# Optimization experiments

Measured on AMD Instinct MI355X. Metric: run time of the kernel, lower is better.

Reference implementation:

```python
import jax, jax.numpy as jnp
import numpy as np

B, T, C, NH = 8, 1024, 1024, 16
DH = C // NH  # 64


def setup_inputs() -> dict:
    key = jax.random.key(0)
    ks = jax.random.split(key, 7)
    s = 1.0 / np.sqrt(C)
    return {
        "x": jax.random.normal(ks[0], (B, T, C), dtype=jnp.float32),
        "Wq": jax.random.normal(ks[1], (C, C), dtype=jnp.float32) * s,
        "bq": jnp.zeros((C,), dtype=jnp.float32),
        "Wk": jax.random.normal(ks[2], (C, C), dtype=jnp.float32) * s,
        "bk": jnp.zeros((C,), dtype=jnp.float32),
        "Wv": jax.random.normal(ks[3], (C, C), dtype=jnp.float32) * s,
        "bv": jnp.zeros((C,), dtype=jnp.float32),
    }


def reference(x, Wq, bq, Wk, bk, Wv, bv):
    # Linear projections (weights stored as [in, out])
    q = x @ Wq + bq  # [B, T, C]
    k = x @ Wk + bk
    v = x @ Wv + bv
    q = q.reshape(B, T, NH, DH)
    k = k.reshape(B, T, NH, DH)
    v = v.reshape(B, T, NH, DH)
    scale = 1.0 / np.sqrt(DH)
    # NOTE: source module's causal mask buffer is all-ones due to a non-inplace
    # masked_fill bug, so attention is NON-causal (mask multiply is a no-op).
    attn = jnp.einsum("bqhd,bkhd->bhqk", q, k) * scale  # [B, NH, T, T]
    attn = jax.nn.softmax(attn, axis=-1)
    # dropout is identity (p=0 / eval)
    o = jnp.einsum("bhqk,bkhd->bqhd", attn, v)  # [B, T, NH, DH]
    return o.reshape(B, T, C)
```

## Files before the change

### kernel.cpp

```cpp
#include <hip/hip_runtime.h>


#define B_  8
#define T_  1024
#define C_  1024
#define NH_ 16
#define DH_ 64
#define M_  (B_ * T_)

typedef __bf16 bf16x8 __attribute__((ext_vector_type(8)));
typedef float  floatx4 __attribute__((ext_vector_type(4)));
typedef float  floatx16 __attribute__((ext_vector_type(16)));
typedef unsigned int uintx4 __attribute__((ext_vector_type(4)));

__device__ __forceinline__ unsigned short f2bf(float f) {
    unsigned int u = __float_as_uint(f);
    unsigned int r = (u + 0x7fffu + ((u >> 16) & 1u)) >> 16;
    return (unsigned short)r;
}

__device__ __forceinline__ unsigned int f2bf2(float a, float b) {
    unsigned int ua = __float_as_uint(a), ub = __float_as_uint(b);
    ua += 0x7fffu + ((ua >> 16) & 1u);
    ub += 0x7fffu + ((ub >> 16) & 1u);
#if __has_builtin(__builtin_amdgcn_perm)
    return __builtin_amdgcn_perm(ub, ua, 0x07060302u);
#else
    return (ua >> 16) | (ub & 0xffff0000u);
#endif
}

__device__ __forceinline__ float fexp2(float x) {
#if __has_builtin(__builtin_amdgcn_exp2f)
    return __builtin_amdgcn_exp2f(x);
#else
    return exp2f(x);
#endif
}

__device__ __forceinline__ void gload_lds16(const void* g, void* l) {
    __builtin_amdgcn_global_load_lds(
        (const __attribute__((address_space(1))) unsigned int*)g,
        (__attribute__((address_space(3))) unsigned int*)l, 16, 0, 0);
}

__global__ __launch_bounds__(256) void prep_kernel(
    const float* __restrict__ x, unsigned short* __restrict__ xb,
    const float* __restrict__ Wq, const float* __restrict__ Wk,
    const float* __restrict__ Wv, unsigned short* __restrict__ WtAll)
{
    int blk = blockIdx.x;
    if (blk < 8192) {
        int i = blk * 256 + threadIdx.x;
        float4 v = ((const float4*)x)[i];
        ushort4 o;
        unsigned int lo = f2bf2(v.x, v.y), hi = f2bf2(v.z, v.w);
        o.x = (unsigned short)lo; o.y = (unsigned short)(lo >> 16);
        o.z = (unsigned short)hi; o.w = (unsigned short)(hi >> 16);
        ((ushort4*)xb)[i] = o;
        return;
    }
    int tb3 = blk - 8192;
    int which = tb3 >> 8;
    int tb = tb3 & 255;
    const float* W = (which == 0) ? Wq : ((which == 1) ? Wk : Wv);
    unsigned short* out = WtAll + (size_t)which * C_ * C_;

    __shared__ __align__(16) unsigned short tile[64 * 68];
    int k0 = (tb >> 4) * 64, n0 = (tb & 15) * 64;
    int c = threadIdx.x & 63, r0 = threadIdx.x >> 6;

    for (int j = 0; j < 16; ++j) {
        int r = r0 + j * 4;
        tile[c * 68 + r] = f2bf(W[(size_t)(k0 + r) * C_ + n0 + c]);
    }
    __syncthreads();
    int k4 = (threadIdx.x & 15) * 4;
    int nw = threadIdx.x >> 4;
    for (int it = 0; it < 4; ++it) {
        int n = nw + it * 16;
        ushort4 o = *(const ushort4*)&tile[n * 68 + k4];
        *(ushort4*)&out[(size_t)(n0 + n) * C_ + k0 + k4] = o;
    }
}

__global__ __launch_bounds__(256, 2) void qkv_gemm_kernel(
    const unsigned short* __restrict__ xb,
    const unsigned short* __restrict__ WtAll,
    const float* __restrict__ bq, const float* __restrict__ bk,
    const float* __restrict__ bv,
    unsigned short* __restrict__ Qb, unsigned short* __restrict__ Kb,
    unsigned short* __restrict__ Vt)
{
    int which = blockIdx.z;
    const unsigned short* W = WtAll + (size_t)which * C_ * C_;
    const float* bias = (which == 0) ? bq : ((which == 1) ? bk : bv);
    float oscale = (which == 0) ? 0.125f * 1.44269504f : 1.0f;

    __shared__ __align__(16) unsigned short As[2][128 * 64];
    __shared__ __align__(16) unsigned short Bs[2][128 * 64];

    int tid = threadIdx.x;
    int wave = tid >> 6, lane = tid & 63;
    int quad = lane >> 4, l16 = lane & 15, l7 = l16 & 7;
    int wm = wave >> 1, wn = wave & 1;
    int bm = blockIdx.x, bn = blockIdx.y;

    floatx4 acc[4][4] = {};

    auto stage = [&](int kt, int bb) {
        #pragma unroll
        for (int i = 0; i < 4; ++i) {
            int c = (wave * 4 + i) * 64 + lane;
            int row = c >> 3;
            int lcol = ((c & 7) ^ (row & 7)) * 8;
            gload_lds16(&xb[(size_t)(bm * 128 + row) * C_ + kt * 64 + lcol],
                        &As[bb][(wave * 4 + i) * 512]);
            gload_lds16(&W[(size_t)(bn * 128 + row) * C_ + kt * 64 + lcol],
                        &Bs[bb][(wave * 4 + i) * 512]);
        }
    };

    stage(0, 0);
    stage(1, 1);
    asm volatile("s_waitcnt vmcnt(8)" ::: "memory");
    __builtin_amdgcn_s_barrier();
    __builtin_amdgcn_sched_barrier(0);

    for (int kt = 0; kt < 16; ++kt) {
        int cur = kt & 1;
        bf16x8 a[2][4], bfr[2][4];
        #pragma unroll
        for (int s = 0; s < 2; ++s) {
            #pragma unroll
            for (int mt = 0; mt < 4; ++mt) {
                int row = wm * 64 + mt * 16 + l16;
                a[s][mt] = *(const bf16x8*)&As[cur][row * 64 + ((s * 4 + quad) ^ l7) * 8];
            }
            #pragma unroll
            for (int nt = 0; nt < 4; ++nt) {
                int row = wn * 64 + nt * 16 + l16;
                bfr[s][nt] = *(const bf16x8*)&Bs[cur][row * 64 + ((s * 4 + quad) ^ l7) * 8];
            }
        }
        asm volatile("s_waitcnt lgkmcnt(0)" ::: "memory");
        __builtin_amdgcn_s_barrier();
        __builtin_amdgcn_sched_barrier(0);

        if (kt + 2 < 16) stage(kt + 2, cur);

        #pragma unroll
        for (int s = 0; s < 2; ++s) {
            if (which < 2) {
                #pragma unroll
                for (int mt = 0; mt < 4; ++mt)
                    #pragma unroll
                    for (int nt = 0; nt < 4; ++nt)
                        acc[mt][nt] = __builtin_amdgcn_mfma_f32_16x16x32_bf16(
                            bfr[s][nt], a[s][mt], acc[mt][nt], 0, 0, 0);
            } else {
                #pragma unroll
                for (int mt = 0; mt < 4; ++mt)
                    #pragma unroll
                    for (int nt = 0; nt < 4; ++nt)
                        acc[mt][nt] = __builtin_amdgcn_mfma_f32_16x16x32_bf16(
                            a[s][mt], bfr[s][nt], acc[mt][nt], 0, 0, 0);
            }
        }

        if (kt < 14) asm volatile("s_waitcnt vmcnt(8)" ::: "memory");
        else         asm volatile("s_waitcnt vmcnt(0)" ::: "memory");
        __builtin_amdgcn_s_barrier();
        __builtin_amdgcn_sched_barrier(0);
    }

    if (which < 2) {
        unsigned short* outp = (which == 0) ? Qb : Kb;
        #pragma unroll
        for (int mt = 0; mt < 4; ++mt) {
            int tg = bm * 128 + wm * 64 + mt * 16 + l16;
            int bb = tg >> 10, t = tg & (T_ - 1);
            #pragma unroll
            for (int nt = 0; nt < 4; ++nt) {
                int colg = bn * 128 + wn * 64 + nt * 16 + quad * 4;
                int h = colg >> 6, d = colg & 63;
                float4 b4 = *(const float4*)&bias[colg];
                uint2 o;
                o.x = f2bf2((acc[mt][nt][0] + b4.x) * oscale,
                            (acc[mt][nt][1] + b4.y) * oscale);
                o.y = f2bf2((acc[mt][nt][2] + b4.z) * oscale,
                            (acc[mt][nt][3] + b4.w) * oscale);
                *(uint2*)&outp[((size_t)(bb * NH_ + h) * T_ + t) * DH_ + d] = o;
            }
        }
    } else {
        int quadp = ((quad & 1) << 1) | (quad >> 1);
        #pragma unroll
        for (int nt = 0; nt < 4; ++nt) {
            int colg = bn * 128 + wn * 64 + nt * 16 + l16;
            int h = colg >> 6, d = colg & 63;
            float bval = bias[colg];
            #pragma unroll
            for (int mt = 0; mt < 4; ++mt) {
                int tg = bm * 128 + wm * 64 + mt * 16 + quadp * 4;
                int bb = tg >> 10, t = tg & (T_ - 1);
                uint2 o;
                o.x = f2bf2(acc[mt][nt][0] + bval, acc[mt][nt][1] + bval);
                o.y = f2bf2(acc[mt][nt][2] + bval, acc[mt][nt][3] + bval);
                *(uint2*)&Vt[((size_t)(bb * NH_ + h) * DH_ + d) * T_ + t] = o;
            }
        }
    }
}

__global__ __launch_bounds__(256) void attn_kernel(
    const unsigned short* __restrict__ Qb,
    const unsigned short* __restrict__ Kb,
    const unsigned short* __restrict__ Vt,
    float* __restrict__ out)
{
    int bh = blockIdx.x;
    int qblk = blockIdx.y;
    int b = bh >> 4, h = bh & (NH_ - 1);
    int tid = threadIdx.x;
    int wave = tid >> 6, lane = tid & 63;
    int l5 = lane & 31, hi = lane >> 5;

    const unsigned short* Qh = Qb + (size_t)bh * T_ * DH_;
    const unsigned short* Kh = Kb + (size_t)bh * T_ * DH_;
    const unsigned short* Vh = Vt + (size_t)bh * DH_ * T_;

    __shared__ __align__(16) unsigned short Ks[2][128 * 64];
    __shared__ __align__(16) unsigned short Vs[2][64 * 128];

    int qrow = qblk * 128 + wave * 32 + l5;
    bf16x8 qa[4];
    #pragma unroll
    for (int sl = 0; sl < 4; ++sl)
        qa[sl] = *(const bf16x8*)&Qh[(size_t)qrow * DH_ + sl * 16 + hi * 8];

    uintx4 ou; ou.x = ou.y = ou.z = ou.w = 0x3F803F80u;
    bf16x8 ones = __builtin_bit_cast(bf16x8, ou);

    floatx16 o_acc[2] = {};
    floatx16 o_sum = {};

    auto stage = [&](int kt2, int bb) {
        #pragma unroll
        for (int i = 0; i < 4; ++i) {
            int c = (wave * 4 + i) * 64 + lane;
            int krow = c >> 3;
            int klcol = ((c & 7) ^ (krow & 7)) * 8;
            gload_lds16(&Kh[(size_t)(kt2 * 128 + krow) * DH_ + klcol],
                        &Ks[bb][(wave * 4 + i) * 512]);
            int vrow = c >> 4;
            int vlcol = ((c & 15) ^ (vrow & 15)) * 8;
            gload_lds16(&Vh[(size_t)vrow * T_ + kt2 * 128 + vlcol],
                        &Vs[bb][(wave * 4 + i) * 512]);
        }
    };

    stage(0, 0);
    for (int kt2 = 0; kt2 < T_ / 128; ++kt2) {
        int cur = kt2 & 1;
        __syncthreads();
        if (kt2 + 1 < T_ / 128) stage(kt2 + 1, cur ^ 1);

        #pragma unroll
        for (int kh = 0; kh < 2; ++kh) {
            #pragma unroll
            for (int nt = 0; nt < 2; ++nt) {
                floatx16 st = {};
                int r = kh * 64 + nt * 32 + l5;
                #pragma unroll
                for (int sl = 0; sl < 4; ++sl) {
                    bf16x8 kb = *(const bf16x8*)&Ks[cur][r * 64 + ((sl * 2 + hi) ^ (r & 7)) * 8];
                    st = __builtin_amdgcn_mfma_f32_32x32x16_bf16(kb, qa[sl], st, 0, 0, 0);
                }

                unsigned int pd[8];
                #pragma unroll
                for (int m = 0; m < 8; ++m) {
                    float e0 = fexp2(st[2 * m]);
                    float e1 = fexp2(st[2 * m + 1]);
                    pd[m] = f2bf2(e0, e1);
                }

                #pragma unroll
                for (int ks2 = 0; ks2 < 2; ++ks2) {
                    uintx4 pbu;
                    pbu.x = pd[ks2 * 4 + 0];
                    pbu.y = pd[ks2 * 4 + 1];
                    pbu.z = pd[ks2 * 4 + 2];
                    pbu.w = pd[ks2 * 4 + 3];
                    bf16x8 pb = __builtin_bit_cast(bf16x8, pbu);
                    o_sum = __builtin_amdgcn_mfma_f32_32x32x16_bf16(
                        ones, pb, o_sum, 0, 0, 0);
                    int ch = kh * 8 + nt * 4 + ks2 * 2 + hi;
                    #pragma unroll
                    for (int dt = 0; dt < 2; ++dt) {
                        int vr = dt * 32 + l5;
                        bf16x8 vb = *(const bf16x8*)&Vs[cur][vr * 128 + (ch ^ (vr & 15)) * 8];
                        o_acc[dt] = __builtin_amdgcn_mfma_f32_32x32x16_bf16(
                            vb, pb, o_acc[dt], 0, 0, 0);
                    }
                }
            }
        }
    }

    float inv = 1.0f / o_sum[0];
    int t = qblk * 128 + wave * 32 + l5;
    float* op = &out[((size_t)b * T_ + t) * C_ + h * DH_];
    #pragma unroll
    for (int dt = 0; dt < 2; ++dt) {
        #pragma unroll
        for (int g = 0; g < 4; ++g) {
            float4 v;
            v.x = o_acc[dt][g * 4 + 0] * inv;
            v.y = o_acc[dt][g * 4 + 1] * inv;
            v.z = o_acc[dt][g * 4 + 2] * inv;
            v.w = o_acc[dt][g * 4 + 3] * inv;
            *(float4*)&op[dt * 32 + g * 8 + hi * 4] = v;
        }
    }
}

extern "C" void kernel_launch(void* const* d_in, const int* in_sizes, int n_in,
                              void* d_out, int out_size, void* d_ws, size_t ws_size,
                              hipStream_t stream) {
    const float* x  = (const float*)d_in[0];
    const float* Wq = (const float*)d_in[1];
    const float* bq = (const float*)d_in[2];
    const float* Wk = (const float*)d_in[3];
    const float* bk = (const float*)d_in[4];
    const float* Wv = (const float*)d_in[5];
    const float* bv = (const float*)d_in[6];
    float* out = (float*)d_out;

    char* ws = (char*)d_ws;
    size_t off = 0;
    unsigned short* xb = (unsigned short*)(ws + off); off += (size_t)M_ * C_ * 2;
    unsigned short* Wt = (unsigned short*)(ws + off); off += (size_t)3 * C_ * C_ * 2;
    unsigned short* Qb = (unsigned short*)(ws + off); off += (size_t)M_ * C_ * 2;
    unsigned short* Kb = (unsigned short*)(ws + off); off += (size_t)M_ * C_ * 2;
    unsigned short* Vt = (unsigned short*)(ws + off); off += (size_t)M_ * C_ * 2;

    prep_kernel<<<dim3(8960), dim3(256), 0, stream>>>(x, xb, Wq, Wk, Wv, Wt);

    qkv_gemm_kernel<<<dim3(M_ / 128, C_ / 128, 3), dim3(256), 0, stream>>>(
        xb, Wt, bq, bk, bv, Qb, Kb, Vt);

    attn_kernel<<<dim3(B_ * NH_, T_ / 128), dim3(256), 0, stream>>>(Qb, Kb, Vt, out);
}
```

Before: 219.0 us.

## Halve QKV GEMM K-tile to raise occupancy; add MFMA priority hints in attention

The QKV projection GEMM drops its K tile from 64 to 32, which halves the LDS footprint. It uses a new two-level XOR swizzle for the 4-chunk rows and raises the launch-bounds occupancy hint from 2 to 4 blocks per CU. The aim is more resident waves to hide global-load latency, at the cost of twice as many barrier-synchronised iterations. Separately, the attention kernel wraps its MFMA sections in s_setprio to favour matrix-issue waves over those doing exp and conversion.

```diff
diff --git a/kernel.cpp b/kernel.cpp
--- a/kernel.cpp
+++ b/kernel.cpp
@@ -84,7 +84,7 @@
     }
 }
 
-__global__ __launch_bounds__(256, 2) void qkv_gemm_kernel(
+__global__ __launch_bounds__(256, 4) void qkv_gemm_kernel(
     const unsigned short* __restrict__ xb,
     const unsigned short* __restrict__ WtAll,
     const float* __restrict__ bq, const float* __restrict__ bk,
@@ -97,12 +97,12 @@
     const float* bias = (which == 0) ? bq : ((which == 1) ? bk : bv);
     float oscale = (which == 0) ? 0.125f * 1.44269504f : 1.0f;
 
-    __shared__ __align__(16) unsigned short As[2][128 * 64];
-    __shared__ __align__(16) unsigned short Bs[2][128 * 64];
+    __shared__ __align__(16) unsigned short As[2][128 * 32];
+    __shared__ __align__(16) unsigned short Bs[2][128 * 32];
 
     int tid = threadIdx.x;
     int wave = tid >> 6, lane = tid & 63;
-    int quad = lane >> 4, l16 = lane & 15, l7 = l16 & 7;
+    int quad = lane >> 4, l16 = lane & 15;
     int wm = wave >> 1, wn = wave & 1;
     int bm = blockIdx.x, bn = blockIdx.y;
 
@@ -110,65 +110,63 @@
 
     auto stage = [&](int kt, int bb) {
         #pragma unroll
-        for (int i = 0; i < 4; ++i) {
-            int c = (wave * 4 + i) * 64 + lane;
-            int row = c >> 3;
-            int lcol = ((c & 7) ^ (row & 7)) * 8;
-            gload_lds16(&xb[(size_t)(bm * 128 + row) * C_ + kt * 64 + lcol],
-                        &As[bb][(wave * 4 + i) * 512]);
-            gload_lds16(&W[(size_t)(bn * 128 + row) * C_ + kt * 64 + lcol],
-                        &Bs[bb][(wave * 4 + i) * 512]);
+        for (int i = 0; i < 2; ++i) {
+            int c = wave * 128 + i * 64 + lane;
+            int row = c >> 2;
+            int lcol = ((c & 3) ^ (row & 3) ^ ((row >> 2) & 3)) * 8;
+            gload_lds16(&xb[(size_t)(bm * 128 + row) * C_ + kt * 32 + lcol],
+                        &As[bb][(wave * 128 + i * 64) * 8]);
+            gload_lds16(&W[(size_t)(bn * 128 + row) * C_ + kt * 32 + lcol],
+                        &Bs[bb][(wave * 128 + i * 64) * 8]);
         }
     };
 
     stage(0, 0);
     stage(1, 1);
-    asm volatile("s_waitcnt vmcnt(8)" ::: "memory");
+    asm volatile("s_waitcnt vmcnt(4)" ::: "memory");
     __builtin_amdgcn_s_barrier();
     __builtin_amdgcn_sched_barrier(0);
 
-    for (int kt = 0; kt < 16; ++kt) {
+    int pc = 0;
+    (void)pc;
+
+    for (int kt = 0; kt < 32; ++kt) {
         int cur = kt & 1;
-        bf16x8 a[2][4], bfr[2][4];
-        #pragma unroll
-        for (int s = 0; s < 2; ++s) {
-            #pragma unroll
-            for (int mt = 0; mt < 4; ++mt) {
-                int row = wm * 64 + mt * 16 + l16;
-                a[s][mt] = *(const bf16x8*)&As[cur][row * 64 + ((s * 4 + quad) ^ l7) * 8];
-            }
-            #pragma unroll
-            for (int nt = 0; nt < 4; ++nt) {
-                int row = wn * 64 + nt * 16 + l16;
-                bfr[s][nt] = *(const bf16x8*)&Bs[cur][row * 64 + ((s * 4 + quad) ^ l7) * 8];
-            }
+        bf16x8 a[4], bfr[4];
+        int xorm = (l16 & 3) ^ ((l16 >> 2) & 3);
+        #pragma unroll
+        for (int mt = 0; mt < 4; ++mt) {
+            int row = wm * 64 + mt * 16 + l16;
+            a[mt] = *(const bf16x8*)&As[cur][row * 32 + (quad ^ xorm) * 8];
+        }
+        #pragma unroll
+        for (int nt = 0; nt < 4; ++nt) {
+            int row = wn * 64 + nt * 16 + l16;
+            bfr[nt] = *(const bf16x8*)&Bs[cur][row * 32 + (quad ^ xorm) * 8];
         }
         asm volatile("s_waitcnt lgkmcnt(0)" ::: "memory");
         __builtin_amdgcn_s_barrier();
         __builtin_amdgcn_sched_barrier(0);
 
-        if (kt + 2 < 16) stage(kt + 2, cur);
-
-        #pragma unroll
-        for (int s = 0; s < 2; ++s) {
-            if (which < 2) {
-                #pragma unroll
-                for (int mt = 0; mt < 4; ++mt)
-                    #pragma unroll
-                    for (int nt = 0; nt < 4; ++nt)
-                        acc[mt][nt] = __builtin_amdgcn_mfma_f32_16x16x32_bf16(
-                            bfr[s][nt], a[s][mt], acc[mt][nt], 0, 0, 0);
-            } else {
-                #pragma unroll
-                for (int mt = 0; mt < 4; ++mt)
-                    #pragma unroll
-                    for (int nt = 0; nt < 4; ++nt)
-                        acc[mt][nt] = __builtin_amdgcn_mfma_f32_16x16x32_bf16(
-                            a[s][mt], bfr[s][nt], acc[mt][nt], 0, 0, 0);
-            }
-        }
-
-        if (kt < 14) asm volatile("s_waitcnt vmcnt(8)" ::: "memory");
+        if (kt + 2 < 32) stage(kt + 2, cur);
+
+        if (which < 2) {
+            #pragma unroll
+            for (int mt = 0; mt < 4; ++mt)
+                #pragma unroll
+                for (int nt = 0; nt < 4; ++nt)
+                    acc[mt][nt] = __builtin_amdgcn_mfma_f32_16x16x32_bf16(
+                        bfr[nt], a[mt], acc[mt][nt], 0, 0, 0);
+        } else {
+            #pragma unroll
+            for (int mt = 0; mt < 4; ++mt)
+                #pragma unroll
+                for (int nt = 0; nt < 4; ++nt)
+                    acc[mt][nt] = __builtin_amdgcn_mfma_f32_16x16x32_bf16(
+                        a[mt], bfr[nt], acc[mt][nt], 0, 0, 0);
+        }
+
+        if (kt < 30) asm volatile("s_waitcnt vmcnt(4)" ::: "memory");
         else         asm volatile("s_waitcnt vmcnt(0)" ::: "memory");
         __builtin_amdgcn_s_barrier();
         __builtin_amdgcn_sched_barrier(0);
@@ -272,11 +270,13 @@
             for (int nt = 0; nt < 2; ++nt) {
                 floatx16 st = {};
                 int r = kh * 64 + nt * 32 + l5;
+                __builtin_amdgcn_s_setprio(1);
                 #pragma unroll
                 for (int sl = 0; sl < 4; ++sl) {
                     bf16x8 kb = *(const bf16x8*)&Ks[cur][r * 64 + ((sl * 2 + hi) ^ (r & 7)) * 8];
                     st = __builtin_amdgcn_mfma_f32_32x32x16_bf16(kb, qa[sl], st, 0, 0, 0);
                 }
+                __builtin_amdgcn_s_setprio(0);
 
                 unsigned int pd[8];
                 #pragma unroll
@@ -286,6 +286,7 @@
                     pd[m] = f2bf2(e0, e1);
                 }
 
+                __builtin_amdgcn_s_setprio(1);
                 #pragma unroll
                 for (int ks2 = 0; ks2 < 2; ++ks2) {
                     uintx4 pbu;
@@ -305,6 +306,7 @@
                             vb, pb, o_acc[dt], 0, 0, 0);
                     }
                 }
+                __builtin_amdgcn_s_setprio(0);
             }
         }
     }
```

Measured after the change: 834.3 us. 3.81x slower.
